# Optimization experiments

Hardware: AMD Instinct MI355X
Metric: run time of the kernel (lower is better)

The kernel has to match this reference:

```python
import jax, jax.numpy as jnp
import numpy as np

# Static problem sizes (must match setup_inputs).
B = 4096      # number of events (unique batch_idx values)
NPER = 2000   # hits per event; NPER == maxhits -> deterministic arange selection
D = 4         # clustering-space dimensionality
EPS = 1e-6


def setup_inputs() -> dict:
    key = jax.random.key(0)
    clust_space = jax.random.normal(key, (B * NPER, D), dtype=jnp.float32)
    # Sorted, equal-sized groups: batch_idx = [0]*NPER, [1]*NPER, ...
    batch_idx = jnp.repeat(jnp.arange(B, dtype=jnp.int32), NPER)
    return {"clust_space": clust_space, "batch_idx": batch_idx}


def reference(clust_space, batch_idx):
    # batch_idx is sorted with equal group sizes, so the per-event Python loop
    # of the original module is a reshape to [B, NPER, D].
    coords = clust_space.reshape(B, NPER, D)
    # Per-event mean and centered coordinates.
    c = coords - coords.mean(axis=1, keepdims=True)            # [B, NPER, D]
    # Covariance: mean over hits of outer products -> [B, D, D] (symmetric).
    cov = jnp.einsum('bnd,bne->bde', c, c) / NPER
    # Symmetric real matrix: eigvalsh == real part of torch.linalg.eig output.
    eig = jnp.linalg.eigvalsh(cov)                             # [B, D]
    pen = jnp.log((eig.mean(axis=-1) / (eig.min(axis=-1) + EPS) - 1.0) ** 2 + 1.0)
    # Original sums the per-event penalties into a scalar loss.
    return pen.sum()
```

## Files before the change

### kernel.cpp

```cpp
#include <hip/hip_runtime.h>
#include <hip/hip_bf16.h>
#include <math.h>

#define NB     4096
#define NPER   2000
#define HALF   1000
#define HALVES (2 * NB)
#define WGS    512
#define WAVES  (WGS * 4)
#define EPS    1e-6

#define ACC(v)                                                             \
    do {                                                                   \
        s0 += (v).x; s1 += (v).y; s2 += (v).z; s3 += (v).w;                \
        m00 += (v).x * (v).x; m01 += (v).x * (v).y;                        \
        m02 += (v).x * (v).z; m03 += (v).x * (v).w;                        \
        m11 += (v).y * (v).y; m12 += (v).y * (v).z; m13 += (v).y * (v).w;  \
        m22 += (v).z * (v).z; m23 += (v).z * (v).w;                        \
        m33 += (v).w * (v).w;                                              \
    } while (0)

__global__ __launch_bounds__(256)
void moments_kernel(const float4* __restrict__ cs, float* __restrict__ mom) {
    const int wave = threadIdx.x >> 6;
    const int lane = threadIdx.x & 63;
    const int w0 = blockIdx.x * 4 + wave;

    for (int e = 0; e < HALVES / WAVES; ++e) {
        const int h = w0 + e * WAVES;
        const float4* __restrict__ p = cs + (size_t)h * HALF;

        float s0 = 0.f, s1 = 0.f, s2 = 0.f, s3 = 0.f;
        float m00 = 0.f, m01 = 0.f, m02 = 0.f, m03 = 0.f;
        float m11 = 0.f, m12 = 0.f, m13 = 0.f;
        float m22 = 0.f, m23 = 0.f, m33 = 0.f;

        float4 v[8];
#pragma unroll
        for (int r = 0; r < 8; ++r) v[r] = p[r * 64 + lane];
#pragma unroll
        for (int r = 0; r < 8; ++r) ACC(v[r]);

#pragma unroll
        for (int r = 0; r < 7; ++r) v[r] = p[512 + r * 64 + lane];
        float4 vt = p[960 + (lane < 40 ? lane : 0)];
        if (lane >= 40) { vt.x = 0.f; vt.y = 0.f; vt.z = 0.f; vt.w = 0.f; }
#pragma unroll
        for (int r = 0; r < 7; ++r) ACC(v[r]);
        ACC(vt);

        float vals[14] = {s0, s1, s2, s3,
                          m00, m01, m02, m03, m11, m12, m13, m22, m23, m33};
#pragma unroll
        for (int j = 0; j < 14; ++j) {
            float x = vals[j];
#pragma unroll
            for (int off = 32; off > 0; off >>= 1)
                x += __shfl_down(x, off, 64);
            vals[j] = x;
        }

        if (lane == 0) {
            float4* o = (float4*)(mom + (size_t)h * 16);
            o[0] = make_float4(vals[0], vals[1], vals[2],  vals[3]);
            o[1] = make_float4(vals[4], vals[5], vals[6],  vals[7]);
            o[2] = make_float4(vals[8], vals[9], vals[10], vals[11]);
            o[3] = make_float4(vals[12], vals[13], 0.f, 0.f);
        }
    }
}

__global__ __launch_bounds__(64)
void pen_kernel(const float* __restrict__ mom, float* __restrict__ out) {
    const int b = blockIdx.x * 64 + threadIdx.x;
    const float* mA = mom + (size_t)(2 * b)     * 16;
    const float* mB = mom + (size_t)(2 * b + 1) * 16;

    double t[14];
#pragma unroll
    for (int j = 0; j < 14; ++j) t[j] = (double)mA[j] + (double)mB[j];

    const double invN = 1.0 / (double)NPER;
    double mu0 = t[0] * invN, mu1 = t[1] * invN,
           mu2 = t[2] * invN, mu3 = t[3] * invN;

    double A[4][4];
    A[0][0] = t[4]  * invN - mu0 * mu0;
    A[0][1] = A[1][0] = t[5]  * invN - mu0 * mu1;
    A[0][2] = A[2][0] = t[6]  * invN - mu0 * mu2;
    A[0][3] = A[3][0] = t[7]  * invN - mu0 * mu3;
    A[1][1] = t[8]  * invN - mu1 * mu1;
    A[1][2] = A[2][1] = t[9]  * invN - mu1 * mu2;
    A[1][3] = A[3][1] = t[10] * invN - mu1 * mu3;
    A[2][2] = t[11] * invN - mu2 * mu2;
    A[2][3] = A[3][2] = t[12] * invN - mu2 * mu3;
    A[3][3] = t[13] * invN - mu3 * mu3;

    for (int sweep = 0; sweep < 8; ++sweep) {
        double off = A[0][1]*A[0][1] + A[0][2]*A[0][2] + A[0][3]*A[0][3]
                   + A[1][2]*A[1][2] + A[1][3]*A[1][3] + A[2][3]*A[2][3];
        if (__all(off < 1e-24)) break;
#pragma unroll
        for (int p = 0; p < 3; ++p) {
#pragma unroll
            for (int q = p + 1; q < 4; ++q) {
                double apq = A[p][q];
                if (fabs(apq) > 1e-300) {
                    double tau = (A[q][q] - A[p][p]) / (2.0 * apq);
                    double tt = (tau >= 0.0 ? 1.0 : -1.0) /
                                (fabs(tau) + sqrt(1.0 + tau * tau));
                    double c = 1.0 / sqrt(1.0 + tt * tt);
                    double s = tt * c;
#pragma unroll
                    for (int k = 0; k < 4; ++k) {
                        double akp = A[k][p], akq = A[k][q];
                        A[k][p] = c * akp - s * akq;
                        A[k][q] = s * akp + c * akq;
                    }
#pragma unroll
                    for (int k = 0; k < 4; ++k) {
                        double apk = A[p][k], aqk = A[q][k];
                        A[p][k] = c * apk - s * aqk;
                        A[q][k] = s * apk + c * aqk;
                    }
                    A[p][q] = 0.0;
                    A[q][p] = 0.0;
                }
            }
        }
    }

    double e0 = A[0][0], e1 = A[1][1], e2 = A[2][2], e3 = A[3][3];
    double mean = 0.25 * (e0 + e1 + e2 + e3);
    double mn = fmin(fmin(e0, e1), fmin(e2, e3));
    double r = mean / (mn + EPS) - 1.0;
    float pen = (float)log(r * r + 1.0);

#pragma unroll
    for (int off = 32; off > 0; off >>= 1)
        pen += __shfl_down(pen, off, 64);
    if (threadIdx.x == 0)
        atomicAdd(out, pen);
}

extern "C" void kernel_launch(void* const* d_in, const int* in_sizes, int n_in,
                              void* d_out, int out_size, void* d_ws, size_t ws_size,
                              hipStream_t stream) {
    const float4* cs = (const float4*)d_in[0];
    float* mom = (float*)d_ws;
    float* out = (float*)d_out;

    hipMemsetAsync(out, 0, sizeof(float), stream);
    moments_kernel<<<WGS, 256, 0, stream>>>(cs, mom);
    pen_kernel<<<NB / 64, 64, 0, stream>>>(mom, out);
}
```

Before: 211.3 us.

## Fuse moments and penalty kernels via grid-wide atomic barrier

Merges the moments and eigen-penalty kernels into a single launch. A global atomic counter acts as a grid barrier, after which 16 blocks compute penalties and a second counter lets block 0 write the final sum. This removes one kernel launch and the gap between launches. It relies on all 512 blocks being co-resident, and the spin-wait adds barrier latency.

```diff
diff --git a/kernel.cpp b/kernel.cpp
--- a/kernel.cpp
+++ b/kernel.cpp
@@ -20,8 +20,15 @@
         m33 += (v).w * (v).w;                                              \
     } while (0)
 
+
 __global__ __launch_bounds__(256)
-void moments_kernel(const float4* __restrict__ cs, float* __restrict__ mom) {
+void fused_kernel(const float4* __restrict__ cs, float* __restrict__ ws,
+                  float* __restrict__ out) {
+    unsigned int* ctr1 = (unsigned int*)ws;
+    float*        loss = ws + 1;
+    unsigned int* ctr2 = (unsigned int*)(ws + 2);
+    float*        mom  = ws + 64;
+
     const int wave = threadIdx.x >> 6;
     const int lane = threadIdx.x & 63;
     const int w0 = blockIdx.x * 4 + wave;
@@ -68,11 +75,22 @@
             o[3] = make_float4(vals[12], vals[13], 0.f, 0.f);
         }
     }
-}
 
-__global__ __launch_bounds__(64)
-void pen_kernel(const float* __restrict__ mom, float* __restrict__ out) {
-    const int b = blockIdx.x * 64 + threadIdx.x;
+    __threadfence();
+    __syncthreads();
+    if (threadIdx.x == 0) {
+        __hip_atomic_fetch_add(ctr1, 1u, __ATOMIC_ACQ_REL,
+                               __HIP_MEMORY_SCOPE_AGENT);
+        while (__hip_atomic_load(ctr1, __ATOMIC_ACQUIRE,
+                                 __HIP_MEMORY_SCOPE_AGENT) < WGS)
+            __builtin_amdgcn_s_sleep(8);
+    }
+    __syncthreads();
+    __threadfence();
+
+    if (blockIdx.x >= 16) return;
+
+    const int b = blockIdx.x * 256 + threadIdx.x;
     const float* mA = mom + (size_t)(2 * b)     * 16;
     const float* mB = mom + (size_t)(2 * b + 1) * 16;
 
@@ -139,18 +157,31 @@
 #pragma unroll
     for (int off = 32; off > 0; off >>= 1)
         pen += __shfl_down(pen, off, 64);
+    if (lane == 0)
+        atomicAdd(loss, pen);
+
+    __threadfence();
+    __syncthreads();
     if (threadIdx.x == 0)
-        atomicAdd(out, pen);
+        __hip_atomic_fetch_add(ctr2, 1u, __ATOMIC_ACQ_REL,
+                               __HIP_MEMORY_SCOPE_AGENT);
+    if (blockIdx.x == 0 && threadIdx.x == 0) {
+        while (__hip_atomic_load(ctr2, __ATOMIC_ACQUIRE,
+                                 __HIP_MEMORY_SCOPE_AGENT) < 16u)
+            __builtin_amdgcn_s_sleep(8);
+        __threadfence();
+        out[0] = __hip_atomic_load(loss, __ATOMIC_ACQUIRE,
+                                   __HIP_MEMORY_SCOPE_AGENT);
+    }
 }
 
 extern "C" void kernel_launch(void* const* d_in, const int* in_sizes, int n_in,
                               void* d_out, int out_size, void* d_ws, size_t ws_size,
                               hipStream_t stream) {
     const float4* cs = (const float4*)d_in[0];
-    float* mom = (float*)d_ws;
+    float* ws  = (float*)d_ws;
     float* out = (float*)d_out;
 
-    hipMemsetAsync(out, 0, sizeof(float), stream);
-    moments_kernel<<<WGS, 256, 0, stream>>>(cs, mom);
-    pen_kernel<<<NB / 64, 64, 0, stream>>>(mom, out);
+    hipMemsetAsync(ws, 0, 16, stream);
+    fused_kernel<<<WGS, 256, 0, stream>>>(cs, ws, out);
 }
```

New measurement: 327.3 us. 1.55x slower.
